# Kernel optimization log

Measured on AMD Instinct MI355X. Metric: run time of the kernel, lower is better.

Reference implementation:

```python
import jax, jax.numpy as jnp
import numpy as np
from math import sqrt

B, S, E, H = 4, 2048, 1024, 16
D = E // H  # per-head dim = 64


def setup_inputs() -> dict:
    key = jax.random.key(0)
    ks = jax.random.split(key, 11)
    f = lambda k, shape, scale=1.0: jax.random.normal(k, shape, dtype=jnp.float32) * scale
    return {
        "Q": f(ks[0], (B, S, E)),
        "K": f(ks[1], (B, S, E)),
        "V": f(ks[2], (B, S, E)),
        "Wq": f(ks[3], (E, E), 1.0 / sqrt(E)),
        "bq": f(ks[4], (E,), 0.02),
        "Wk": f(ks[5], (E, E), 1.0 / sqrt(E)),
        "bk": f(ks[6], (E,), 0.02),
        "Wv": f(ks[7], (E, E), 1.0 / sqrt(E)),
        "bv": f(ks[8], (E,), 0.02),
        "Wo": f(ks[9], (E, E), 1.0 / sqrt(E)),
        "bo": f(ks[10], (E,), 0.02),
    }


def reference(Q, K, V, Wq, bq, Wk, bk, Wv, bv, Wo, bo):
    # Linear projections (torch Linear: x @ W.T + b)
    q = Q @ Wq.T + bq  # [B,S,E]
    k = K @ Wk.T + bk
    v = V @ Wv.T + bv
    # torch.chunk along last dim into H heads == reshape [B,S,H,D]
    q = q.reshape(B, S, H, D)
    k = k.reshape(B, S, H, D)
    v = v.reshape(B, S, H, D)
    scale = 1.0 / sqrt(D)
    # batched-over-heads scaled dot-product attention
    scores = jnp.einsum("bqhd,bkhd->bhqk", q, k) * scale  # [B,H,S,S]
    attn = jax.nn.softmax(scores, axis=-1)
    out = jnp.einsum("bhqk,bkhd->bqhd", attn, v).reshape(B, S, E)
    # dropout p=0.0 -> identity
    return out @ Wo.T + bo
```

## Files before the change

### kernel.cpp

```cpp
#include <hip/hip_runtime.h>
#include <hip/hip_bf16.h>

#define B_SZ   4
#define S_LEN  2048
#define E_DIM  1024
#define H_NUM  16
#define D_DIM  64
#define M_ROWS (B_SZ * S_LEN)
#define QK_SCALE 0.1803368801111204f

typedef __attribute__((ext_vector_type(8))) __bf16 bf16x8;
typedef __attribute__((ext_vector_type(4))) float  f32x4;

__device__ __forceinline__ bf16x8 load8(const void* p) {
    return __builtin_bit_cast(bf16x8, *reinterpret_cast<const uint4*>(p));
}

#if defined(__has_builtin)
#if __has_builtin(__builtin_amdgcn_exp2f)
#define EXP2F(x) __builtin_amdgcn_exp2f(x)
#endif
#if __has_builtin(__builtin_amdgcn_global_load_lds)
#define HAVE_GLL 1
#endif
#endif
#ifndef EXP2F
#define EXP2F(x) exp2f(x)
#endif

__device__ __forceinline__ void stage16(const __hip_bfloat16* g, __hip_bfloat16* lbase, int lane) {
#ifdef HAVE_GLL
    __builtin_amdgcn_global_load_lds((const __attribute__((address_space(1))) unsigned int*)g,
                                     (__attribute__((address_space(3))) unsigned int*)lbase,
                                     16, 0, 0);
#else
    reinterpret_cast<uint4*>(lbase)[lane] = *reinterpret_cast<const uint4*>(g);
#endif
}

__global__ __launch_bounds__(256) void cvt_f32_bf16(const float* __restrict__ s,
                                                    __hip_bfloat16* __restrict__ d,
                                                    int n8)
{
    const int i = blockIdx.x * 256 + threadIdx.x;
    if (i >= n8) return;
    const float4 a = reinterpret_cast<const float4*>(s)[i * 2];
    const float4 b = reinterpret_cast<const float4*>(s)[i * 2 + 1];
    __hip_bfloat16 o[8];
    o[0] = __float2bfloat16(a.x); o[1] = __float2bfloat16(a.y);
    o[2] = __float2bfloat16(a.z); o[3] = __float2bfloat16(a.w);
    o[4] = __float2bfloat16(b.x); o[5] = __float2bfloat16(b.y);
    o[6] = __float2bfloat16(b.z); o[7] = __float2bfloat16(b.w);
    reinterpret_cast<uint4*>(d)[i] = *reinterpret_cast<uint4*>(o);
}

struct GemmArgs {
    const __hip_bfloat16* A[3];
    const __hip_bfloat16* W[3];
    const float* bias[3];
    void* C[3];
    float scale[3];
    int mode[3];
};

__global__ __launch_bounds__(512, 4) void gemm_bt(GemmArgs g)
{
    __shared__ __attribute__((aligned(16))) char lds_raw[3 * 24576];

    const int tid = threadIdx.x;
    const int wid = tid >> 6, lane = tid & 63;
    const int quad = lane >> 4, l16 = lane & 15;
    const int wm = wid >> 2, wn = wid & 3;

    const int seg = blockIdx.x >> 8;
    int bid = blockIdx.x & 255;
    bid = (bid & 7) * 32 + (bid >> 3);
    const int bm = bid >> 2, bn = bid & 3;
    const int row0 = bm * 128, col0 = bn * 256;

    const __hip_bfloat16* A = g.A[seg];
    const __hip_bfloat16* W = g.W[seg];

    const int s_line = tid >> 3, s_gr = tid & 7;
    const int glin  = s_gr ^ (s_line & 7);
    const int s_row = (s_line << 1) + (glin >> 2);
    const int s_ks  = glin & 3;
    const __hip_bfloat16* gA = A + (size_t)(row0 + s_row) * E_DIM + s_ks * 8;
    const __hip_bfloat16* gB = W + (size_t)(col0 + s_row) * E_DIM + s_ks * 8;
    const int stA = wid << 10;

    const int rg   = (((l16 & 1) << 2) | quad) ^ ((l16 >> 1) & 7);
    const int aoff = (wm * 32 + (l16 >> 1)) * 128 + rg * 16;
    const int boff = (wn * 32 + (l16 >> 1)) * 128 + rg * 16;

    f32x4 acc[4][4];
    const f32x4 zero = {0.f, 0.f, 0.f, 0.f};
#pragma unroll
    for (int i = 0; i < 4; i++)
#pragma unroll
        for (int j = 0; j < 4; j++) acc[i][j] = zero;

    auto stage_t = [&](int t) {
        char* b = lds_raw + (t % 3) * 24576;
        const int ko = t * 32;
        stage16(gA + ko, (__hip_bfloat16*)(b + stA), lane);
        stage16(gB + ko, (__hip_bfloat16*)(b + 8192 + stA), lane);
        stage16(gB + (size_t)128 * E_DIM + ko, (__hip_bfloat16*)(b + 16384 + stA), lane);
    };

    auto body = [&](int t, bool stg) {
        __builtin_amdgcn_s_barrier();
        __builtin_amdgcn_sched_barrier(0);
        if (stg) stage_t(t + 2);
        const char* ab = lds_raw + (t % 3) * 24576;
        bf16x8 af[4], bf[4];
#pragma unroll
        for (int i = 0; i < 4; i++) af[i] = load8(ab + aoff + i * 1024);
#pragma unroll
        for (int j = 0; j < 4; j++) bf[j] = load8(ab + 8192 + boff + j * 1024);
        __builtin_amdgcn_s_setprio(1);
#pragma unroll
        for (int i = 0; i < 4; i++)
#pragma unroll
            for (int j = 0; j < 4; j++)
                acc[i][j] = __builtin_amdgcn_mfma_f32_16x16x32_bf16(af[i], bf[j], acc[i][j], 0, 0, 0);
        __builtin_amdgcn_s_setprio(0);
        __builtin_amdgcn_sched_barrier(0);
    };

    const int NT = E_DIM / 32;
    stage_t(0); stage_t(1);
    for (int t = 0; t < NT - 2; ++t) {
        asm volatile("s_waitcnt vmcnt(3)" ::: "memory");
        body(t, true);
    }
    asm volatile("s_waitcnt vmcnt(3)" ::: "memory"); body(NT - 2, false);
    asm volatile("s_waitcnt vmcnt(0)" ::: "memory"); body(NT - 1, false);

    const int   mode  = g.mode[seg];
    const float scale = g.scale[seg];
    const float* bias = g.bias[seg];
    void* Cout        = g.C[seg];
#pragma unroll
    for (int j = 0; j < 4; j++) {
        const int col = col0 + wn * 64 + j * 16 + l16;
        const float bv = bias[col];
#pragma unroll
        for (int i = 0; i < 4; i++) {
            const int row = row0 + wm * 64 + i * 16 + quad * 4;
            if (mode == 3) {
                __attribute__((aligned(8))) __hip_bfloat16 o[4];
#pragma unroll
                for (int r = 0; r < 4; r++) o[r] = __float2bfloat16((acc[i][j][r] + bv) * scale);
                const int b_ = row >> 11, s_ = row & 2047, h_ = col >> 6, d_ = col & 63;
                *reinterpret_cast<uint2*>((__hip_bfloat16*)Cout +
                    (((size_t)(b_ * H_NUM + h_)) << 17) + (d_ << 11) + s_) =
                    *reinterpret_cast<uint2*>(o);
            } else {
#pragma unroll
                for (int r = 0; r < 4; r++) {
                    const float v = (acc[i][j][r] + bv) * scale;
                    const int rr = row + r;
                    if (mode == 0) {
                        ((__hip_bfloat16*)Cout)[(size_t)rr * E_DIM + col] = __float2bfloat16(v);
                    } else if (mode == 1) {
                        ((float*)Cout)[(size_t)rr * E_DIM + col] = v;
                    } else {
                        const int b_ = rr >> 11, s_ = rr & 2047, h_ = col >> 6, d_ = col & 63;
                        ((__hip_bfloat16*)Cout)[(((size_t)(b_ * H_NUM + h_)) << 17) + (s_ << 6) + d_] =
                            __float2bfloat16(v);
                    }
                }
            }
        }
    }
}

__global__ __launch_bounds__(256) void attn(const __hip_bfloat16* __restrict__ Qt,
                                            const __hip_bfloat16* __restrict__ Kt,
                                            const __hip_bfloat16* __restrict__ Vt,
                                            __hip_bfloat16* __restrict__ Op)
{
    __shared__ __hip_bfloat16 Pls[4][64][40];

    const int x = blockIdx.x;
    const int xcd = x & 7, idx = x >> 3;
    const int bh     = xcd * 8 + (idx & 7);
    const int qchunk = idx >> 3;
    const int wave = threadIdx.x >> 6, lane = threadIdx.x & 63;
    const int quad = lane >> 4, l16 = lane & 15;
    const int qrow0 = qchunk * 256 + wave * 64;

    const __hip_bfloat16* qb = Qt + ((size_t)bh << 17);
    const __hip_bfloat16* kb = Kt + ((size_t)bh << 17);
    const __hip_bfloat16* vb = Vt + ((size_t)bh << 17);
    __hip_bfloat16* pw = &Pls[wave][0][0];

    bf16x8 qf[4][2];
#pragma unroll
    for (int qt = 0; qt < 4; qt++) {
        qf[qt][0] = load8(qb + ((qrow0 + qt * 16 + l16) << 6) + quad * 8);
        qf[qt][1] = load8(qb + ((qrow0 + qt * 16 + l16) << 6) + 32 + quad * 8);
    }

    const f32x4 zero = {0.f, 0.f, 0.f, 0.f};
    f32x4 o_acc[4][4];
#pragma unroll
    for (int qt = 0; qt < 4; qt++)
#pragma unroll
        for (int dj = 0; dj < 4; dj++) o_acc[qt][dj] = zero;
    float lsum[4] = {0.f, 0.f, 0.f, 0.f};

    bf16x8 kaA[2], kcA[2], vfA[4], kaB[2], kcB[2], vfB[4];

    auto prefetch = [&](bf16x8 (&ka)[2], bf16x8 (&kc)[2], bf16x8 (&vf)[4], int kv) {
#pragma unroll
        for (int t = 0; t < 2; t++) {
            ka[t] = load8(kb + ((kv + t * 16 + l16) << 6) + quad * 8);
            kc[t] = load8(kb + ((kv + t * 16 + l16) << 6) + 32 + quad * 8);
        }
#pragma unroll
        for (int dj = 0; dj < 4; dj++)
            vf[dj] = load8(vb + ((size_t)(dj * 16 + l16) << 11) + kv + quad * 8);
    };

    auto compute = [&](const bf16x8 (&ka)[2], const bf16x8 (&kc)[2], const bf16x8 (&vf)[4]) {
#pragma unroll
        for (int t = 0; t < 2; t++) {
#pragma unroll
            for (int qt = 0; qt < 4; qt++) {
                f32x4 st = __builtin_amdgcn_mfma_f32_16x16x32_bf16(ka[t], qf[qt][0], zero, 0, 0, 0);
                st       = __builtin_amdgcn_mfma_f32_16x16x32_bf16(kc[t], qf[qt][1], st, 0, 0, 0);
                const float p0 = EXP2F(st[0]), p1 = EXP2F(st[1]);
                const float p2 = EXP2F(st[2]), p3 = EXP2F(st[3]);
                lsum[qt] += (p0 + p1) + (p2 + p3);
                const unsigned u0 = (unsigned)__bfloat16_as_ushort(__float2bfloat16(p0));
                const unsigned u1 = (unsigned)__bfloat16_as_ushort(__float2bfloat16(p1));
                const unsigned u2 = (unsigned)__bfloat16_as_ushort(__float2bfloat16(p2));
                const unsigned u3 = (unsigned)__bfloat16_as_ushort(__float2bfloat16(p3));
                uint2 w;
                w.x = (u1 << 16) | u0;
                w.y = (u3 << 16) | u2;
                *reinterpret_cast<uint2*>(&pw[(qt * 16 + l16) * 40 + t * 16 + quad * 4]) = w;
            }
        }
        __builtin_amdgcn_s_setprio(1);
#pragma unroll
        for (int qt = 0; qt < 4; qt++) {
            const bf16x8 pa = load8(&pw[(qt * 16 + l16) * 40 + quad * 8]);
#pragma unroll
            for (int dj = 0; dj < 4; dj++)
                o_acc[qt][dj] = __builtin_amdgcn_mfma_f32_16x16x32_bf16(pa, vf[dj], o_acc[qt][dj], 0, 0, 0);
        }
        __builtin_amdgcn_s_setprio(0);
    };

    prefetch(kaA, kcA, vfA, 0);
    for (int kv0 = 0; kv0 < S_LEN; kv0 += 64) {
        prefetch(kaB, kcB, vfB, (kv0 + 32) & (S_LEN - 1));
        __builtin_amdgcn_sched_barrier(0);
        compute(kaA, kcA, vfA);
        prefetch(kaA, kcA, vfA, (kv0 + 64) & (S_LEN - 1));
        __builtin_amdgcn_sched_barrier(0);
        compute(kaB, kcB, vfB);
    }

    const int b_ = bh >> 4, h_ = bh & 15;
#pragma unroll
    for (int qt = 0; qt < 4; qt++) {
        float l = lsum[qt];
        l += __shfl_xor(l, 16, 64);
        l += __shfl_xor(l, 32, 64);
#pragma unroll
        for (int r = 0; r < 4; r++) {
            const float lr = __shfl(l, quad * 4 + r, 64);
            const float inv = 1.f / lr;
            const size_t ro = ((size_t)b_ * S_LEN + (qrow0 + qt * 16 + quad * 4 + r)) * E_DIM + h_ * D_DIM;
#pragma unroll
            for (int dj = 0; dj < 4; dj++)
                Op[ro + dj * 16 + l16] = __float2bfloat16(o_acc[qt][dj][r] * inv);
        }
    }
}

extern "C" void kernel_launch(void* const* d_in, const int* in_sizes, int n_in,
                              void* d_out, int out_size, void* d_ws, size_t ws_size,
                              hipStream_t stream)
{
    const float* Qf  = (const float*)d_in[0];
    const float* Kf  = (const float*)d_in[1];
    const float* Vf  = (const float*)d_in[2];
    const float* Wqf = (const float*)d_in[3];
    const float* bqf = (const float*)d_in[4];
    const float* Wkf = (const float*)d_in[5];
    const float* bkf = (const float*)d_in[6];
    const float* Wvf = (const float*)d_in[7];
    const float* bvf = (const float*)d_in[8];
    const float* Wof = (const float*)d_in[9];
    const float* bof = (const float*)d_in[10];

    const size_t n_act = (size_t)M_ROWS * E_DIM;
    const size_t n_w   = (size_t)E_DIM * E_DIM;

    const dim3 blk(256), gblk(512);
    const int cg_act = (int)(n_act / 8 / 256);
    const int cg_w   = (int)(n_w / 8 / 256);

    const size_t need_fast = (6 * n_act + 4 * n_w) * sizeof(__hip_bfloat16);

    if (ws_size >= need_fast) {
        __hip_bfloat16* Xq = (__hip_bfloat16*)d_ws;
        __hip_bfloat16* Xk = Xq + n_act;
        __hip_bfloat16* Xv = Xk + n_act;
        __hip_bfloat16* Wb = Xv + n_act;
        __hip_bfloat16* Qt = Wb + 4 * n_w;
        __hip_bfloat16* Kt = Qt + n_act;
        __hip_bfloat16* Vt = Kt + n_act;

        cvt_f32_bf16<<<cg_act, blk, 0, stream>>>(Qf,  Xq,          (int)(n_act / 8));
        cvt_f32_bf16<<<cg_act, blk, 0, stream>>>(Kf,  Xk,          (int)(n_act / 8));
        cvt_f32_bf16<<<cg_act, blk, 0, stream>>>(Vf,  Xv,          (int)(n_act / 8));
        cvt_f32_bf16<<<cg_w,   blk, 0, stream>>>(Wqf, Wb,          (int)(n_w / 8));
        cvt_f32_bf16<<<cg_w,   blk, 0, stream>>>(Wkf, Wb + n_w,    (int)(n_w / 8));
        cvt_f32_bf16<<<cg_w,   blk, 0, stream>>>(Wvf, Wb + 2*n_w,  (int)(n_w / 8));
        cvt_f32_bf16<<<cg_w,   blk, 0, stream>>>(Wof, Wb + 3*n_w,  (int)(n_w / 8));

        GemmArgs qkv;
        qkv.A[0] = Xq;  qkv.A[1] = Xk;  qkv.A[2] = Xv;
        qkv.W[0] = Wb;  qkv.W[1] = Wb + n_w;  qkv.W[2] = Wb + 2*n_w;
        qkv.bias[0] = bqf;  qkv.bias[1] = bkf;  qkv.bias[2] = bvf;
        qkv.C[0] = Qt;  qkv.C[1] = Kt;  qkv.C[2] = Vt;
        qkv.scale[0] = QK_SCALE;  qkv.scale[1] = 1.0f;  qkv.scale[2] = 1.0f;
        qkv.mode[0] = 2;  qkv.mode[1] = 2;  qkv.mode[2] = 3;
        gemm_bt<<<dim3(768), gblk, 0, stream>>>(qkv);

        attn<<<dim3(512), blk, 0, stream>>>(Qt, Kt, Vt, Xq);

        GemmArgs og;
        og.A[0] = Xq;  og.A[1] = Xq;  og.A[2] = Xq;
        og.W[0] = Wb + 3*n_w;  og.W[1] = og.W[0];  og.W[2] = og.W[0];
        og.bias[0] = bof;  og.bias[1] = bof;  og.bias[2] = bof;
        og.C[0] = d_out;  og.C[1] = d_out;  og.C[2] = d_out;
        og.scale[0] = 1.0f;  og.scale[1] = 1.0f;  og.scale[2] = 1.0f;
        og.mode[0] = 1;  og.mode[1] = 1;  og.mode[2] = 1;
        gemm_bt<<<dim3(256), gblk, 0, stream>>>(og);
    } else {
        __hip_bfloat16* X  = (__hip_bfloat16*)d_ws;
        __hip_bfloat16* Wb = X + n_act;
        __hip_bfloat16* Qt = Wb + n_w;
        __hip_bfloat16* Kt = Qt + n_act;
        __hip_bfloat16* Vt = Kt + n_act;

        auto one = [&](const float* Af, const float* Wf, const float* bf_,
                       void* C, float sc, int md) {
            cvt_f32_bf16<<<cg_act, blk, 0, stream>>>(Af, X, (int)(n_act / 8));
            cvt_f32_bf16<<<cg_w,   blk, 0, stream>>>(Wf, Wb, (int)(n_w / 8));
            GemmArgs a;
            a.A[0] = X; a.A[1] = X; a.A[2] = X;
            a.W[0] = Wb; a.W[1] = Wb; a.W[2] = Wb;
            a.bias[0] = bf_; a.bias[1] = bf_; a.bias[2] = bf_;
            a.C[0] = C; a.C[1] = C; a.C[2] = C;
            a.scale[0] = sc; a.scale[1] = sc; a.scale[2] = sc;
            a.mode[0] = md; a.mode[1] = md; a.mode[2] = md;
            gemm_bt<<<dim3(256), gblk, 0, stream>>>(a);
        };
        one(Qf, Wqf, bqf, Qt, QK_SCALE, 2);
        one(Kf, Wkf, bkf, Kt, 1.0f, 2);
        one(Vf, Wvf, bvf, Vt, 1.0f, 3);
        attn<<<dim3(512), blk, 0, stream>>>(Qt, Kt, Vt, X);
        cvt_f32_bf16<<<cg_w, blk, 0, stream>>>(Wof, Wb, (int)(n_w / 8));
        GemmArgs og;
        og.A[0] = X; og.A[1] = X; og.A[2] = X;
        og.W[0] = Wb; og.W[1] = Wb; og.W[2] = Wb;
        og.bias[0] = bof; og.bias[1] = bof; og.bias[2] = bof;
        og.C[0] = d_out; og.C[1] = d_out; og.C[2] = d_out;
        og.scale[0] = 1.0f; og.scale[1] = 1.0f; og.scale[2] = 1.0f;
        og.mode[0] = 1; og.mode[1] = 1; og.mode[2] = 1;
        gemm_bt<<<dim3(256), gblk, 0, stream>>>(og);
    }
}
```

Before: 379.5 us.

## Split attention KV range across two wave groups and retile GEMM to four waves

The attention kernel now runs 8 waves per block. Each half of the waves processes half of the key/value sequence for the same query rows, then the partial outputs and row sums are combined through LDS before the write-out. This targets low occupancy, since the grid has only 512 blocks. The projection GEMM moves from 8 waves with 64x64 tiles each to 4 waves with 128x64 tiles each, which raises per-wave register use and A-fragment reuse and adjusts staging and waitcnt depths. The merge adds synchronisation and LDS traffic, and it is only correct if both halves share a common softmax max reference.

```diff
diff --git a/kernel.cpp b/kernel.cpp
--- a/kernel.cpp
+++ b/kernel.cpp
@@ -63,14 +63,13 @@
     int mode[3];
 };
 
-__global__ __launch_bounds__(512, 4) void gemm_bt(GemmArgs g)
+__global__ __launch_bounds__(256, 2) void gemm_bt(GemmArgs g)
 {
     __shared__ __attribute__((aligned(16))) char lds_raw[3 * 24576];
 
     const int tid = threadIdx.x;
     const int wid = tid >> 6, lane = tid & 63;
     const int quad = lane >> 4, l16 = lane & 15;
-    const int wm = wid >> 2, wn = wid & 3;
 
     const int seg = blockIdx.x >> 8;
     int bid = blockIdx.x & 255;
@@ -85,27 +84,29 @@
     const int glin  = s_gr ^ (s_line & 7);
     const int s_row = (s_line << 1) + (glin >> 2);
     const int s_ks  = glin & 3;
-    const __hip_bfloat16* gA = A + (size_t)(row0 + s_row) * E_DIM + s_ks * 8;
-    const __hip_bfloat16* gB = W + (size_t)(col0 + s_row) * E_DIM + s_ks * 8;
-    const int stA = wid << 10;
+    const __hip_bfloat16* gA0 = A + (size_t)(row0 + s_row) * E_DIM + s_ks * 8;
+    const __hip_bfloat16* gB0 = W + (size_t)(col0 + s_row) * E_DIM + s_ks * 8;
+    const int stW = wid << 10;
 
     const int rg   = (((l16 & 1) << 2) | quad) ^ ((l16 >> 1) & 7);
-    const int aoff = (wm * 32 + (l16 >> 1)) * 128 + rg * 16;
-    const int boff = (wn * 32 + (l16 >> 1)) * 128 + rg * 16;
-
-    f32x4 acc[4][4];
+    const int rbase = (l16 >> 1) * 128 + rg * 16;
+
+    f32x4 acc[8][4];
     const f32x4 zero = {0.f, 0.f, 0.f, 0.f};
 #pragma unroll
-    for (int i = 0; i < 4; i++)
+    for (int i = 0; i < 8; i++)
 #pragma unroll
         for (int j = 0; j < 4; j++) acc[i][j] = zero;
 
     auto stage_t = [&](int t) {
         char* b = lds_raw + (t % 3) * 24576;
         const int ko = t * 32;
-        stage16(gA + ko, (__hip_bfloat16*)(b + stA), lane);
-        stage16(gB + ko, (__hip_bfloat16*)(b + 8192 + stA), lane);
-        stage16(gB + (size_t)128 * E_DIM + ko, (__hip_bfloat16*)(b + 16384 + stA), lane);
+        stage16(gA0 + ko,                          (__hip_bfloat16*)(b + stW), lane);
+        stage16(gA0 + (size_t)64 * E_DIM + ko,     (__hip_bfloat16*)(b + 4096 + stW), lane);
+        char* bB = b + 8192;
+#pragma unroll
+        for (int c = 0; c < 4; c++)
+            stage16(gB0 + (size_t)(64 * c) * E_DIM + ko, (__hip_bfloat16*)(bB + c * 4096 + stW), lane);
     };
 
     auto body = [&](int t, bool stg) {
@@ -113,14 +114,14 @@
         __builtin_amdgcn_sched_barrier(0);
         if (stg) stage_t(t + 2);
         const char* ab = lds_raw + (t % 3) * 24576;
-        bf16x8 af[4], bf[4];
-#pragma unroll
-        for (int i = 0; i < 4; i++) af[i] = load8(ab + aoff + i * 1024);
-#pragma unroll
-        for (int j = 0; j < 4; j++) bf[j] = load8(ab + 8192 + boff + j * 1024);
+        bf16x8 af[8], bf[4];
+#pragma unroll
+        for (int i = 0; i < 8; i++) af[i] = load8(ab + rbase + i * 1024);
+#pragma unroll
+        for (int j = 0; j < 4; j++) bf[j] = load8(ab + 8192 + wid * 4096 + rbase + j * 1024);
         __builtin_amdgcn_s_setprio(1);
 #pragma unroll
-        for (int i = 0; i < 4; i++)
+        for (int i = 0; i < 8; i++)
 #pragma unroll
             for (int j = 0; j < 4; j++)
                 acc[i][j] = __builtin_amdgcn_mfma_f32_16x16x32_bf16(af[i], bf[j], acc[i][j], 0, 0, 0);
@@ -131,10 +132,10 @@
     const int NT = E_DIM / 32;
     stage_t(0); stage_t(1);
     for (int t = 0; t < NT - 2; ++t) {
-        asm volatile("s_waitcnt vmcnt(3)" ::: "memory");
+        asm volatile("s_waitcnt vmcnt(6)" ::: "memory");
         body(t, true);
     }
-    asm volatile("s_waitcnt vmcnt(3)" ::: "memory"); body(NT - 2, false);
+    asm volatile("s_waitcnt vmcnt(6)" ::: "memory"); body(NT - 2, false);
     asm volatile("s_waitcnt vmcnt(0)" ::: "memory"); body(NT - 1, false);
 
     const int   mode  = g.mode[seg];
@@ -143,11 +144,11 @@
     void* Cout        = g.C[seg];
 #pragma unroll
     for (int j = 0; j < 4; j++) {
-        const int col = col0 + wn * 64 + j * 16 + l16;
+        const int col = col0 + wid * 64 + j * 16 + l16;
         const float bv = bias[col];
 #pragma unroll
-        for (int i = 0; i < 4; i++) {
-            const int row = row0 + wm * 64 + i * 16 + quad * 4;
+        for (int i = 0; i < 8; i++) {
+            const int row = row0 + i * 16 + quad * 4;
             if (mode == 3) {
                 __attribute__((aligned(8))) __hip_bfloat16 o[4];
 #pragma unroll
@@ -176,12 +177,12 @@
     }
 }
 
-__global__ __launch_bounds__(256) void attn(const __hip_bfloat16* __restrict__ Qt,
-                                            const __hip_bfloat16* __restrict__ Kt,
-                                            const __hip_bfloat16* __restrict__ Vt,
-                                            __hip_bfloat16* __restrict__ Op)
+__global__ __launch_bounds__(512, 4) void attn(const __hip_bfloat16* __restrict__ Qt,
+                                               const __hip_bfloat16* __restrict__ Kt,
+                                               const __hip_bfloat16* __restrict__ Vt,
+                                               __hip_bfloat16* __restrict__ Op)
 {
-    __shared__ __hip_bfloat16 Pls[4][64][40];
+    __shared__ __attribute__((aligned(16))) __hip_bfloat16 Pls[8][64][40];
 
     const int x = blockIdx.x;
     const int xcd = x & 7, idx = x >> 3;
@@ -189,7 +190,9 @@
     const int qchunk = idx >> 3;
     const int wave = threadIdx.x >> 6, lane = threadIdx.x & 63;
     const int quad = lane >> 4, l16 = lane & 15;
-    const int qrow0 = qchunk * 256 + wave * 64;
+    const int rw = wave & 3, kshalf = wave >> 2;
+    const int qrow0 = qchunk * 256 + rw * 64;
+    const int kvbase = kshalf << 10;
 
     const __hip_bfloat16* qb = Qt + ((size_t)bh << 17);
     const __hip_bfloat16* kb = Kt + ((size_t)bh << 17);
@@ -255,8 +258,8 @@
         __builtin_amdgcn_s_setprio(0);
     };
 
-    prefetch(kaA, kcA, vfA, 0);
-    for (int kv0 = 0; kv0 < S_LEN; kv0 += 64) {
+    prefetch(kaA, kcA, vfA, kvbase);
+    for (int kv0 = kvbase; kv0 < kvbase + 1024; kv0 += 64) {
         prefetch(kaB, kcB, vfB, (kv0 + 32) & (S_LEN - 1));
         __builtin_amdgcn_sched_barrier(0);
         compute(kaA, kcA, vfA);
@@ -264,6 +267,37 @@
         __builtin_amdgcn_sched_barrier(0);
         compute(kaB, kcB, vfB);
     }
+
+    float* mb = reinterpret_cast<float*>(&Pls[0][0][0]);
+    __syncthreads();
+#pragma unroll
+    for (int ph = 0; ph < 2; ph++) {
+        if (kshalf == 1) {
+#pragma unroll
+            for (int q2 = 0; q2 < 2; q2++) {
+                const int qt = ph * 2 + q2;
+#pragma unroll
+                for (int dj = 0; dj < 4; dj++)
+                    *reinterpret_cast<f32x4*>(&mb[(((rw * 2 + q2) * 4 + dj) << 8) + (lane << 2)]) = o_acc[qt][dj];
+                mb[8192 + (rw * 2 + q2) * 64 + lane] = lsum[qt];
+            }
+        }
+        __syncthreads();
+        if (kshalf == 0) {
+#pragma unroll
+            for (int q2 = 0; q2 < 2; q2++) {
+                const int qt = ph * 2 + q2;
+#pragma unroll
+                for (int dj = 0; dj < 4; dj++) {
+                    const f32x4 v = *reinterpret_cast<const f32x4*>(&mb[(((rw * 2 + q2) * 4 + dj) << 8) + (lane << 2)]);
+                    o_acc[qt][dj] += v;
+                }
+                lsum[qt] += mb[8192 + (rw * 2 + q2) * 64 + lane];
+            }
+        }
+        __syncthreads();
+    }
+    if (kshalf == 1) return;
 
     const int b_ = bh >> 4, h_ = bh & 15;
 #pragma unroll
@@ -302,7 +336,7 @@
     const size_t n_act = (size_t)M_ROWS * E_DIM;
     const size_t n_w   = (size_t)E_DIM * E_DIM;
 
-    const dim3 blk(256), gblk(512);
+    const dim3 blk(256), gblk(256), ablk(512);
     const int cg_act = (int)(n_act / 8 / 256);
     const int cg_w   = (int)(n_w / 8 / 256);
 
@@ -334,7 +368,7 @@
         qkv.mode[0] = 2;  qkv.mode[1] = 2;  qkv.mode[2] = 3;
         gemm_bt<<<dim3(768), gblk, 0, stream>>>(qkv);
 
-        attn<<<dim3(512), blk, 0, stream>>>(Qt, Kt, Vt, Xq);
+        attn<<<dim3(512), ablk, 0, stream>>>(Qt, Kt, Vt, Xq);
 
         GemmArgs og;
         og.A[0] = Xq;  og.A[1] = Xq;  og.A[2] = Xq;
@@ -367,7 +401,7 @@
         one(Qf, Wqf, bqf, Qt, QK_SCALE, 2);
         one(Kf, Wkf, bkf, Kt, 1.0f, 2);
         one(Vf, Wvf, bvf, Vt, 1.0f, 3);
-        attn<<<dim3(512), blk, 0, stream>>>(Qt, Kt, Vt, X);
+        attn<<<dim3(512), ablk, 0, stream>>>(Qt, Kt, Vt, X);
         cvt_f32_bf16<<<cg_w, blk, 0, stream>>>(Wof, Wb, (int)(n_w / 8));
         GemmArgs og;
         og.A[0] = X; og.A[1] = X; og.A[2] = X;
```

New measurement: 1.276 ms. 236% more time.
